# Kernel tuning notes

Hardware: AMD Instinct MI355X
Metric: run time of the kernel (lower is better)

Reference implementation:

```python
import jax, jax.numpy as jnp
import numpy as np

N0, N1, N2 = 20000, 15000, 15000
N = N0 + N1 + N2          # total nodes
E = 800000                # edges
H, D = 4, 64              # heads, hidden per head
ED = 64                   # edge feature dim
NET = 8                   # num edge types
C = 16                    # num classes
SLOPE = 0.2               # leaky relu negative slope
ALPHA = 0.05              # residual-attention mixing

def _glorot(key, shape):
    return jax.random.normal(key, shape, dtype=jnp.float32) / jnp.sqrt(jnp.float32(shape[-1]))

def setup_inputs() -> dict:
    key = jax.random.key(0)
    ks = jax.random.split(key, 32)
    return {
        "x0": jax.random.normal(ks[0], (N0, 128), jnp.float32),
        "x1": jax.random.normal(ks[1], (N1, 64), jnp.float32),
        "x2": jax.random.normal(ks[2], (N2, 32), jnp.float32),
        "src": jax.random.randint(ks[3], (E,), 0, N),
        "dst": jax.random.randint(ks[4], (E,), 0, N),
        "efeat": jax.random.randint(ks[5], (E,), 0, NET),
        # per-node-type input projections (fc_list)
        "W0": _glorot(ks[6], (64, 128)), "b0": jnp.zeros((64,), jnp.float32),
        "W1": _glorot(ks[7], (64, 64)),  "b1": jnp.zeros((64,), jnp.float32),
        "W2": _glorot(ks[8], (64, 32)),  "b2": jnp.zeros((64,), jnp.float32),
        # GAT layer 0: in 64 -> H*D, no residual, elu
        "Wg0": _glorot(ks[9], (H * D, 64)),
        "etab0": _glorot(ks[10], (NET, ED)),
        "We0": _glorot(ks[11], (H * ED, ED)),
        "al0": _glorot(ks[12], (H, D)), "ar0": _glorot(ks[13], (H, D)), "ae0": _glorot(ks[14], (H, ED)),
        # GAT layer 1: in H*D -> H*D, identity residual, elu
        "Wg1": _glorot(ks[15], (H * D, H * D)),
        "etab1": _glorot(ks[16], (NET, ED)),
        "We1": _glorot(ks[17], (H * ED, ED)),
        "al1": _glorot(ks[18], (H, D)), "ar1": _glorot(ks[19], (H, D)), "ae1": _glorot(ks[20], (H, ED)),
        # final GAT layer: in H*D -> 1*C, linear residual, no activation
        "Wg2": _glorot(ks[21], (C, H * D)),
        "etab2": _glorot(ks[22], (NET, ED)),
        "We2": _glorot(ks[23], (ED, ED)),
        "al2": _glorot(ks[24], (1, C)), "ar2": _glorot(ks[25], (1, C)), "ae2": _glorot(ks[26], (1, ED)),
        "resW2": _glorot(ks[27], (C, H * D)),
    }

def _edge_softmax(scores, dst):
    # softmax over incoming edges of each dst node; scores: [E, H]
    m = jax.ops.segment_max(scores, dst, num_segments=N)
    ex = jnp.exp(scores - m[dst])
    s = jax.ops.segment_sum(ex, dst, num_segments=N)
    return ex / (s[dst] + 1e-9)

def _gat_conv(h, src, dst, et, Wg, etab, We, al, ar, ae, res_attn, res, resW, act):
    nH, oD = al.shape
    feat = (h @ Wg.T).reshape(N, nH, oD)                 # [N,H,D]
    ee = (etab[et] @ We.T).reshape(E, nH, -1)            # [E,H,ED]
    el = jnp.einsum('nhd,hd->nh', feat, al)
    er = jnp.einsum('nhd,hd->nh', feat, ar)
    es = jnp.einsum('ehd,hd->eh', ee, ae)
    logits = jax.nn.leaky_relu(el[src] + er[dst] + es, SLOPE)
    a = _edge_softmax(logits, dst)                       # [E,H]
    if res_attn is not None:
        a = a * (1.0 - ALPHA) + res_attn * ALPHA
    out = jax.ops.segment_sum(a[:, :, None] * feat[src], dst, num_segments=N)
    if res:
        resval = (h @ resW.T).reshape(N, -1, oD) if resW is not None else h.reshape(N, nH, oD)
        out = out + resval
    if act is not None:
        out = act(out)
    return out, jax.lax.stop_gradient(a)                 # attention detached (res_attn)

def reference(x0, x1, x2, src, dst, efeat, W0, b0, W1, b1, W2, b2,
              Wg0, etab0, We0, al0, ar0, ae0,
              Wg1, etab1, We1, al1, ar1, ae1,
              Wg2, etab2, We2, al2, ar2, ae2, resW2):
    h = jnp.concatenate([x0 @ W0.T + b0, x1 @ W1.T + b1, x2 @ W2.T + b2], axis=0)  # [N,64]
    h, ra = _gat_conv(h, src, dst, efeat, Wg0, etab0, We0, al0, ar0, ae0, None, False, None, jax.nn.elu)
    h = h.reshape(N, -1)
    h, ra = _gat_conv(h, src, dst, efeat, Wg1, etab1, We1, al1, ar1, ae1, ra, True, None, jax.nn.elu)
    h = h.reshape(N, -1)
    logits, _ = _gat_conv(h, src, dst, efeat, Wg2, etab2, We2, al2, ar2, ae2, None, True, resW2, None)
    return logits.mean(axis=1)                           # [N, C]
```

## Files before the change

### kernel.cpp

```cpp
#include <hip/hip_runtime.h>
#include <math.h>

#define N0 20000
#define N1 15000
#define N2 15000
#define NN 50000
#define EE 800000
#define SLOPE 0.2f
#define ALPHA 0.05f

typedef _Float16 h8 __attribute__((ext_vector_type(8)));
typedef _Float16 h4 __attribute__((ext_vector_type(4)));
typedef float f4v __attribute__((ext_vector_type(4)));

__device__ __forceinline__ float sel4(float4 v, int h) {
    float lo = (h & 1) ? v.y : v.x;
    float hi = (h & 1) ? v.w : v.z;
    return (h & 2) ? hi : lo;
}

__device__ __forceinline__ float elu_fast(float x) {
    return x > 0.f ? x : __expf(x) - 1.f;
}


__device__ __forceinline__ void es_pair(int p,
                                        const float* __restrict__ etab0, const float* __restrict__ We0, const float* __restrict__ ae0,
                                        const float* __restrict__ etab1, const float* __restrict__ We1, const float* __restrict__ ae1,
                                        const float* __restrict__ etab2, const float* __restrict__ We2, const float* __restrict__ ae2,
                                        float* __restrict__ es) {
    const float *etab, *We, *ae;
    float* out;
    int H;
    if (p < 32)      { etab = etab0; We = We0; ae = ae0; out = es;      H = 4; }
    else if (p < 64) { p -= 32; etab = etab1; We = We1; ae = ae1; out = es + 32; H = 4; }
    else             { p -= 64; etab = etab2; We = We2; ae = ae2; out = es + 64; H = 1; }
    int t = p / H, h = p % H;
    int j = threadIdx.x & 63;
    const float* w = We + (size_t)(h * 64 + j) * 64;
    const float* e = etab + t * 64;
    float s = 0.f;
    #pragma unroll
    for (int k = 0; k < 64; k += 4) {
        float4 wv = *(const float4*)(w + k);
        float4 ev = *(const float4*)(e + k);
        s += wv.x * ev.x + wv.y * ev.y + wv.z * ev.z + wv.w * ev.w;
    }
    s *= ae[h * 64 + j];
    #pragma unroll
    for (int off = 32; off > 0; off >>= 1) s += __shfl_down(s, off);
    if (j == 0) out[t * H + h] = s;
}

__device__ __forceinline__ void cvt4(const float* __restrict__ s, _Float16* __restrict__ d, int t) {
    float4 v = ((const float4*)s)[t];
    h4 o;
    o[0] = (_Float16)v.x; o[1] = (_Float16)v.y;
    o[2] = (_Float16)v.z; o[3] = (_Float16)v.w;
    ((h4*)d)[t] = o;
}


__global__ __launch_bounds__(256) void k1_hist_prep(
        const int* __restrict__ dst, int* __restrict__ deg,
        const float* etab0, const float* We0, const float* ae0,
        const float* etab1, const float* We1, const float* ae1,
        const float* etab2, const float* We2, const float* ae2,
        float* es,
        const float* s0, _Float16* d0, int n0,
        const float* s1, _Float16* d1, int n1,
        const float* s2, _Float16* d2, int n2,
        const float* s3, _Float16* d3, int n3,
        const float* s4, _Float16* d4, int n4,
        const float* s5, _Float16* d5, int n5,
        const float* s6, _Float16* d6, int n6,
        const float* s7, _Float16* d7, int n7,
        const float* s8, _Float16* d8, int n8,
        const float* s9, _Float16* d9, int n9, int EB) {
    int b = blockIdx.x;
    if (b < EB) {
        int e = b * 256 + threadIdx.x;
        if (e < EE) atomicAdd(&deg[dst[e]], 1);
        return;
    }
    b -= EB;
    if (b < 18) {
        int p = b * 4 + (threadIdx.x >> 6);
        if (p < 72) es_pair(p, etab0, We0, ae0, etab1, We1, ae1, etab2, We2, ae2, es);
        return;
    }
    int t = (b - 18) * 256 + threadIdx.x;
    if (t < (n0 >> 2)) { cvt4(s0, d0, t); return; } t -= n0 >> 2;
    if (t < (n1 >> 2)) { cvt4(s1, d1, t); return; } t -= n1 >> 2;
    if (t < (n2 >> 2)) { cvt4(s2, d2, t); return; } t -= n2 >> 2;
    if (t < (n3 >> 2)) { cvt4(s3, d3, t); return; } t -= n3 >> 2;
    if (t < (n4 >> 2)) { cvt4(s4, d4, t); return; } t -= n4 >> 2;
    if (t < (n5 >> 2)) { cvt4(s5, d5, t); return; } t -= n5 >> 2;
    if (t < (n6 >> 2)) { cvt4(s6, d6, t); return; } t -= n6 >> 2;
    if (t < (n7 >> 2)) { cvt4(s7, d7, t); return; } t -= n7 >> 2;
    if (t < (n8 >> 2)) { cvt4(s8, d8, t); return; } t -= n8 >> 2;
    if (t < (n9 >> 2)) { cvt4(s9, d9, t); }
}


__device__ __forceinline__ void block_sum_body(int b, const int* __restrict__ deg,
                                               int* __restrict__ bsum, int n) {
    int i = b * 256 + threadIdx.x;
    int v = (i < n) ? deg[i] : 0;
    #pragma unroll
    for (int off = 32; off > 0; off >>= 1) v += __shfl_down(v, off);
    __shared__ int sh[4];
    if ((threadIdx.x & 63) == 0) sh[threadIdx.x >> 6] = v;
    __syncthreads();
    if (threadIdx.x == 0) bsum[b] = sh[0] + sh[1] + sh[2] + sh[3];
}

__global__ __launch_bounds__(256) void scan_out2(const int* __restrict__ deg,
                                                 const int* __restrict__ bsum,
                                                 int* __restrict__ rowstart,
                                                 int* __restrict__ cursor, int n, int nb) {
    __shared__ int sb[256];
    __shared__ int boff_s;
    int tid = threadIdx.x;
    int v = (tid < nb) ? bsum[tid] : 0;
    sb[tid] = v;
    __syncthreads();
    #pragma unroll
    for (int off = 1; off < 256; off <<= 1) {
        int t = (tid >= off) ? sb[tid - off] : 0;
        __syncthreads();
        sb[tid] += t;
        __syncthreads();
    }
    if (tid == blockIdx.x) boff_s = sb[tid] - v;
    __syncthreads();
    int boff = boff_s;
    int i = blockIdx.x * 256 + tid;
    int d = (i < n) ? deg[i] : 0;
    __syncthreads();
    sb[tid] = d;
    __syncthreads();
    #pragma unroll
    for (int off = 1; off < 256; off <<= 1) {
        int t = (tid >= off) ? sb[tid - off] : 0;
        __syncthreads();
        sb[tid] += t;
        __syncthreads();
    }
    int excl = sb[tid] - d + boff;
    if (i < n) { rowstart[i] = excl; cursor[i] = excl; }
    if (i == n - 1) rowstart[n] = excl + d;
}


template<int NT, int ELR>
__device__ __forceinline__ void gemm_body(int bx, int by,
                                          const _Float16* __restrict__ A,
                                          const _Float16* __restrict__ B,
                                          const float* __restrict__ bias,
                                          float* __restrict__ Cf,
                                          _Float16* __restrict__ Ch,
                                          float* __restrict__ el,
                                          float* __restrict__ er,
                                          const float* __restrict__ al,
                                          const float* __restrict__ ar,
                                          int M, int N, int K) {
    const int wave = threadIdx.x >> 6;
    const int lane = threadIdx.x & 63;
    const int m_base = (bx * 4 + wave) * 32;
    const int n_base = by * (NT * 16);
    const int row = lane & 15;
    const int kq = (lane >> 4) * 8;

    f4v acc[2][NT];
    #pragma unroll
    for (int i = 0; i < 2; i++)
        #pragma unroll
        for (int j = 0; j < NT; j++) {
            f4v z = {0.f, 0.f, 0.f, 0.f};
            acc[i][j] = z;
        }

    int ra = m_base + row;       if (ra >= M) ra = M - 1;
    int rb2 = m_base + 16 + row; if (rb2 >= M) rb2 = M - 1;
    const _Float16* a0p = A + (size_t)ra * K + kq;
    const _Float16* a1p = A + (size_t)rb2 * K + kq;
    const _Float16* bp  = B + (size_t)(n_base + row) * K + kq;

    for (int k = 0; k < K; k += 32) {
        h8 a0 = *(const h8*)(a0p + k);
        h8 a1 = *(const h8*)(a1p + k);
        #pragma unroll
        for (int j = 0; j < NT; j++) {
            h8 b = *(const h8*)(bp + (size_t)j * 16 * K + k);
            acc[0][j] = __builtin_amdgcn_mfma_f32_16x16x32_f16(a0, b, acc[0][j], 0, 0, 0);
            acc[1][j] = __builtin_amdgcn_mfma_f32_16x16x32_f16(a1, b, acc[1][j], 0, 0, 0);
        }
    }

    const int col = lane & 15;
    const int rb = (lane >> 4) * 4;

    if (ELR == 1) {
        float alw[NT], arw[NT];
        #pragma unroll
        for (int j = 0; j < NT; j++) {
            int cg = n_base + j * 16 + col;
            int hg = cg >> 6, d = cg & 63;
            alw[j] = al[hg * 64 + d];
            arw[j] = ar[hg * 64 + d];
        }
        const int hb = n_base >> 6;
        #pragma unroll
        for (int ms = 0; ms < 2; ms++) {
            #pragma unroll
            for (int r = 0; r < 4; r++) {
                float e0 = 0.f, e1 = 0.f, f0 = 0.f, f1 = 0.f;
                #pragma unroll
                for (int j = 0; j < NT; j++) {
                    float av = acc[ms][j][r];
                    if (j < NT / 2) { e0 = fmaf(av, alw[j], e0); f0 = fmaf(av, arw[j], f0); }
                    else            { e1 = fmaf(av, alw[j], e1); f1 = fmaf(av, arw[j], f1); }
                }
                #pragma unroll
                for (int off = 1; off <= 8; off <<= 1) {
                    e0 += __shfl_xor(e0, off);
                    e1 += __shfl_xor(e1, off);
                    f0 += __shfl_xor(f0, off);
                    f1 += __shfl_xor(f1, off);
                }
                int m = m_base + ms * 16 + rb + r;
                if (col == 0 && m < M) {
                    el[m * 4 + hb]     = e0;
                    el[m * 4 + hb + 1] = e1;
                    er[m * 4 + hb]     = f0;
                    er[m * 4 + hb + 1] = f1;
                }
            }
        }
    }
    if (ELR == 2) {
        float alw = al[col], arw = ar[col];
        #pragma unroll
        for (int ms = 0; ms < 2; ms++) {
            #pragma unroll
            for (int r = 0; r < 4; r++) {
                float e = acc[ms][0][r] * alw;
                float f = acc[ms][0][r] * arw;
                #pragma unroll
                for (int off = 1; off <= 8; off <<= 1) {
                    e += __shfl_xor(e, off);
                    f += __shfl_xor(f, off);
                }
                int m = m_base + ms * 16 + rb + r;
                if (col == 0 && m < M) { el[m] = e; er[m] = f; }
            }
        }
    }

    #pragma unroll
    for (int ms = 0; ms < 2; ms++) {
        #pragma unroll
        for (int j = 0; j < NT; j++) {
            #pragma unroll
            for (int r = 0; r < 4; r++) {
                int m = m_base + ms * 16 + rb + r;
                if (m < M) {
                    int n = n_base + j * 16 + col;
                    float v = acc[ms][j][r];
                    if (bias) v += bias[n];
                    if (Cf) Cf[(size_t)m * N + n] = v;
                    if (Ch) Ch[(size_t)m * N + n] = (_Float16)v;
                }
            }
        }
    }
}

template<int NT, int ELR>
__global__ __launch_bounds__(256) void gemm_mfma(const _Float16* __restrict__ A,
                                                 const _Float16* __restrict__ B,
                                                 const float* __restrict__ bias,
                                                 float* __restrict__ Cf,
                                                 _Float16* __restrict__ Ch,
                                                 float* __restrict__ el,
                                                 float* __restrict__ er,
                                                 const float* __restrict__ al,
                                                 const float* __restrict__ ar,
                                                 int M, int N, int K) {
    gemm_body<NT, ELR>(blockIdx.x, blockIdx.y, A, B, bias, Cf, Ch, el, er, al, ar, M, N, K);
}


__global__ __launch_bounds__(256) void k2_bsum_proj(
        const int* __restrict__ deg, int* __restrict__ bsum, int NBv,
        const _Float16* __restrict__ x0h, const _Float16* __restrict__ W0h, const float* __restrict__ b0,
        const _Float16* __restrict__ x1h, const _Float16* __restrict__ W1h, const float* __restrict__ b1,
        const _Float16* __restrict__ x2h, const _Float16* __restrict__ W2h, const float* __restrict__ b2,
        _Float16* __restrict__ h0h, int nb0, int nb1) {
    int b = blockIdx.x;
    if (b < NBv) { block_sum_body(b, deg, bsum, NN); return; }
    b -= NBv;
    if (b < nb0) {
        gemm_body<4, 0>(b, 0, x0h, W0h, b0, nullptr, h0h,
                        nullptr, nullptr, nullptr, nullptr, N0, 64, 128);
    } else if (b < nb0 + nb1) {
        gemm_body<4, 0>(b - nb0, 0, x1h, W1h, b1, nullptr, h0h + (size_t)N0 * 64,
                        nullptr, nullptr, nullptr, nullptr, N1, 64, 64);
    } else {
        gemm_body<4, 0>(b - nb0 - nb1, 0, x2h, W2h, b2, nullptr, h0h + (size_t)(N0 + N1) * 64,
                        nullptr, nullptr, nullptr, nullptr, N2, 64, 32);
    }
}


__global__ __launch_bounds__(256) void k4_scat_gemm0(
        const int* __restrict__ src, const int* __restrict__ dst, const int* __restrict__ et,
        int* __restrict__ cursor, int* __restrict__ pk, int EB,
        const _Float16* __restrict__ h0h, const _Float16* __restrict__ Wg0h,
        _Float16* __restrict__ feath, float* __restrict__ el, float* __restrict__ er,
        const float* __restrict__ al0, const float* __restrict__ ar0, int MB) {
    int b = blockIdx.x;
    if (b < EB) {
        int e = b * 256 + threadIdx.x;
        if (e < EE) {
            int d = dst[e];
            int p = atomicAdd(&cursor[d], 1);
            pk[p] = (et[e] << 16) | src[e];
        }
        return;
    }
    int t = b - EB;
    int bx = t % MB, by = t / MB;
    gemm_body<8, 1>(bx, by, h0h, Wg0h, nullptr, nullptr, feath, el, er, al0, ar0, NN, 256, 64);
}


template<bool WRITE_A, bool HAS_PREV, bool HAS_RES>
__global__ __launch_bounds__(256) void gat_fused4(const int* __restrict__ rowstart,
                                                  const int* __restrict__ pk,
                                                  const float* __restrict__ el,
                                                  const float* __restrict__ er,
                                                  const float* __restrict__ es,
                                                  const _Float16* __restrict__ feat,
                                                  const _Float16* __restrict__ aprev,
                                                  _Float16* __restrict__ awrite,
                                                  const _Float16* __restrict__ resh,
                                                  _Float16* __restrict__ outh, int nN) {
    __shared__ int2 as_lds[4][4][66];
    const int wave = threadIdx.x >> 6;
    const int lane = threadIdx.x & 63;
    int n = blockIdx.x * 4 + wave;
    if (n >= nN) return;
    const int r0 = rowstart[n], r1 = rowstart[n + 1];
    const int deg = r1 - r0;
    float4 er4 = *(const float4*)(er + n * 4);

    if (deg <= 64) {
        const int idx = r0 + lane;
        const bool act = idx < r1;
        int p = act ? pk[idx] : 0;
        int psrc = p & 0xFFFF;
        float4 v4 = {-INFINITY, -INFINITY, -INFINITY, -INFINITY};
        if (act) {
            float4 e4 = *(const float4*)(el + psrc * 4);
            float4 c4 = *(const float4*)(es + (p >> 16) * 4);
            float v;
            v = e4.x + er4.x + c4.x; v4.x = v > 0.f ? v : SLOPE * v;
            v = e4.y + er4.y + c4.y; v4.y = v > 0.f ? v : SLOPE * v;
            v = e4.z + er4.z + c4.z; v4.z = v > 0.f ? v : SLOPE * v;
            v = e4.w + er4.w + c4.w; v4.w = v > 0.f ? v : SLOPE * v;
        }
        float4 m4 = v4;
        #pragma unroll
        for (int off = 1; off <= 8; off <<= 1) {
            m4.x = fmaxf(m4.x, __shfl_xor(m4.x, off));
            m4.y = fmaxf(m4.y, __shfl_xor(m4.y, off));
            m4.z = fmaxf(m4.z, __shfl_xor(m4.z, off));
            m4.w = fmaxf(m4.w, __shfl_xor(m4.w, off));
        }
        if (deg > 16) {
            m4.x = fmaxf(m4.x, __shfl_xor(m4.x, 16));
            m4.y = fmaxf(m4.y, __shfl_xor(m4.y, 16));
            m4.z = fmaxf(m4.z, __shfl_xor(m4.z, 16));
            m4.w = fmaxf(m4.w, __shfl_xor(m4.w, 16));
        }
        if (deg > 32) {
            m4.x = fmaxf(m4.x, __shfl_xor(m4.x, 32));
            m4.y = fmaxf(m4.y, __shfl_xor(m4.y, 32));
            m4.z = fmaxf(m4.z, __shfl_xor(m4.z, 32));
            m4.w = fmaxf(m4.w, __shfl_xor(m4.w, 32));
        }
        float4 ex = {0.f, 0.f, 0.f, 0.f};
        if (act) {
            ex.x = __expf(v4.x - m4.x);
            ex.y = __expf(v4.y - m4.y);
            ex.z = __expf(v4.z - m4.z);
            ex.w = __expf(v4.w - m4.w);
        }
        float4 s4 = ex;
        #pragma unroll
        for (int off = 1; off <= 8; off <<= 1) {
            s4.x += __shfl_xor(s4.x, off);
            s4.y += __shfl_xor(s4.y, off);
            s4.z += __shfl_xor(s4.z, off);
            s4.w += __shfl_xor(s4.w, off);
        }
        if (deg > 16) {
            s4.x += __shfl_xor(s4.x, 16);
            s4.y += __shfl_xor(s4.y, 16);
            s4.z += __shfl_xor(s4.z, 16);
            s4.w += __shfl_xor(s4.w, 16);
        }
        if (deg > 32) {
            s4.x += __shfl_xor(s4.x, 32);
            s4.y += __shfl_xor(s4.y, 32);
            s4.z += __shfl_xor(s4.z, 32);
            s4.w += __shfl_xor(s4.w, 32);
        }
        float4 a4;
        a4.x = ex.x / (s4.x + 1e-9f);
        a4.y = ex.y / (s4.y + 1e-9f);
        a4.z = ex.z / (s4.z + 1e-9f);
        a4.w = ex.w / (s4.w + 1e-9f);
        if (HAS_PREV && act) {
            h4 pv = *(const h4*)(aprev + (size_t)idx * 4);
            a4.x = a4.x * (1.f - ALPHA) + ALPHA * (float)pv[0];
            a4.y = a4.y * (1.f - ALPHA) + ALPHA * (float)pv[1];
            a4.z = a4.z * (1.f - ALPHA) + ALPHA * (float)pv[2];
            a4.w = a4.w * (1.f - ALPHA) + ALPHA * (float)pv[3];
        }
        if (WRITE_A && act) {
            h4 aw;
            aw[0] = (_Float16)a4.x; aw[1] = (_Float16)a4.y;
            aw[2] = (_Float16)a4.z; aw[3] = (_Float16)a4.w;
            *(h4*)(awrite + (size_t)idx * 4) = aw;
        }
        as_lds[wave][0][lane] = make_int2(__float_as_int(a4.x), psrc);
        as_lds[wave][1][lane] = make_int2(__float_as_int(a4.y), psrc);
        as_lds[wave][2][lane] = make_int2(__float_as_int(a4.z), psrc);
        as_lds[wave][3][lane] = make_int2(__float_as_int(a4.w), psrc);

        const int half = lane >> 5;
        const int fl = lane & 31;
        const int h = fl >> 3;
        float acc8[8];
        #pragma unroll
        for (int q = 0; q < 8; q++) acc8[q] = 0.f;
        int i = r0;
        for (; i + 7 < r1; i += 8) {
            int j0 = (i - r0) + half;
            int2 e0 = as_lds[wave][h][j0 + 0];
            int2 e1 = as_lds[wave][h][j0 + 2];
            int2 e2 = as_lds[wave][h][j0 + 4];
            int2 e3 = as_lds[wave][h][j0 + 6];
            float a0 = __int_as_float(e0.x), a1 = __int_as_float(e1.x);
            float a2 = __int_as_float(e2.x), a3 = __int_as_float(e3.x);
            h8 f0 = *(const h8*)(feat + (size_t)e0.y * 256 + fl * 8);
            h8 f1 = *(const h8*)(feat + (size_t)e1.y * 256 + fl * 8);
            h8 f2 = *(const h8*)(feat + (size_t)e2.y * 256 + fl * 8);
            h8 f3 = *(const h8*)(feat + (size_t)e3.y * 256 + fl * 8);
            #pragma unroll
            for (int q = 0; q < 8; q++) acc8[q] = fmaf(a0, (float)f0[q], acc8[q]);
            #pragma unroll
            for (int q = 0; q < 8; q++) acc8[q] = fmaf(a1, (float)f1[q], acc8[q]);
            #pragma unroll
            for (int q = 0; q < 8; q++) acc8[q] = fmaf(a2, (float)f2[q], acc8[q]);
            #pragma unroll
            for (int q = 0; q < 8; q++) acc8[q] = fmaf(a3, (float)f3[q], acc8[q]);
        }
        for (; i + 3 < r1; i += 4) {
            int j0 = (i - r0) + half;
            int2 e0 = as_lds[wave][h][j0 + 0];
            int2 e1 = as_lds[wave][h][j0 + 2];
            float a0 = __int_as_float(e0.x), a1 = __int_as_float(e1.x);
            h8 f0 = *(const h8*)(feat + (size_t)e0.y * 256 + fl * 8);
            h8 f1 = *(const h8*)(feat + (size_t)e1.y * 256 + fl * 8);
            #pragma unroll
            for (int q = 0; q < 8; q++) acc8[q] = fmaf(a0, (float)f0[q], acc8[q]);
            #pragma unroll
            for (int q = 0; q < 8; q++) acc8[q] = fmaf(a1, (float)f1[q], acc8[q]);
        }
        for (; i + 1 < r1; i += 2) {
            int j0 = (i - r0) + half;
            int2 e0 = as_lds[wave][h][j0];
            float a0 = __int_as_float(e0.x);
            h8 f0 = *(const h8*)(feat + (size_t)e0.y * 256 + fl * 8);
            #pragma unroll
            for (int q = 0; q < 8; q++) acc8[q] = fmaf(a0, (float)f0[q], acc8[q]);
        }
        if (i < r1) {
            int j0 = i - r0;
            int2 e0 = as_lds[wave][h][j0];
            float a0 = (half == 0) ? __int_as_float(e0.x) : 0.f;
            h8 f0 = *(const h8*)(feat + (size_t)e0.y * 256 + fl * 8);
            #pragma unroll
            for (int q = 0; q < 8; q++) acc8[q] = fmaf(a0, (float)f0[q], acc8[q]);
        }
        #pragma unroll
        for (int q = 0; q < 8; q++) acc8[q] += __shfl_xor(acc8[q], 32);

        if (half == 0) {
            if (HAS_RES) {
                h8 rv = *(const h8*)(resh + (size_t)n * 256 + fl * 8);
                #pragma unroll
                for (int q = 0; q < 8; q++) acc8[q] += (float)rv[q];
            }
            #pragma unroll
            for (int q = 0; q < 8; q++) acc8[q] = elu_fast(acc8[q]);
            h8 o;
            #pragma unroll
            for (int q = 0; q < 8; q++) o[q] = (_Float16)acc8[q];
            *(h8*)(outh + (size_t)n * 256 + fl * 8) = o;
        }
        return;
    }

    float4 m4 = {-INFINITY, -INFINITY, -INFINITY, -INFINITY};
    for (int base = r0; base < r1; base += 64) {
        int idx = base + lane;
        if (idx < r1) {
            int p = pk[idx];
            float4 e4 = *(const float4*)(el + (p & 0xFFFF) * 4);
            float4 c4 = *(const float4*)(es + (p >> 16) * 4);
            float v;
            v = e4.x + er4.x + c4.x; v = v > 0.f ? v : SLOPE * v; m4.x = fmaxf(m4.x, v);
            v = e4.y + er4.y + c4.y; v = v > 0.f ? v : SLOPE * v; m4.y = fmaxf(m4.y, v);
            v = e4.z + er4.z + c4.z; v = v > 0.f ? v : SLOPE * v; m4.z = fmaxf(m4.z, v);
            v = e4.w + er4.w + c4.w; v = v > 0.f ? v : SLOPE * v; m4.w = fmaxf(m4.w, v);
        }
    }
    #pragma unroll
    for (int off = 1; off < 64; off <<= 1) {
        m4.x = fmaxf(m4.x, __shfl_xor(m4.x, off));
        m4.y = fmaxf(m4.y, __shfl_xor(m4.y, off));
        m4.z = fmaxf(m4.z, __shfl_xor(m4.z, off));
        m4.w = fmaxf(m4.w, __shfl_xor(m4.w, off));
    }
    float4 s4 = {0.f, 0.f, 0.f, 0.f};
    for (int base = r0; base < r1; base += 64) {
        int idx = base + lane;
        if (idx < r1) {
            int p = pk[idx];
            float4 e4 = *(const float4*)(el + (p & 0xFFFF) * 4);
            float4 c4 = *(const float4*)(es + (p >> 16) * 4);
            float4 exv;
            float v;
            v = e4.x + er4.x + c4.x; v = v > 0.f ? v : SLOPE * v; exv.x = __expf(v - m4.x);
            v = e4.y + er4.y + c4.y; v = v > 0.f ? v : SLOPE * v; exv.y = __expf(v - m4.y);
            v = e4.z + er4.z + c4.z; v = v > 0.f ? v : SLOPE * v; exv.z = __expf(v - m4.z);
            v = e4.w + er4.w + c4.w; v = v > 0.f ? v : SLOPE * v; exv.w = __expf(v - m4.w);
            if (base == r0) {
                as_lds[wave][0][lane] = make_int2(__float_as_int(exv.x), p & 0xFFFF);
                as_lds[wave][1][lane] = make_int2(__float_as_int(exv.y), p & 0xFFFF);
                as_lds[wave][2][lane] = make_int2(__float_as_int(exv.z), p & 0xFFFF);
                as_lds[wave][3][lane] = make_int2(__float_as_int(exv.w), p & 0xFFFF);
            }
            s4.x += exv.x; s4.y += exv.y; s4.z += exv.z; s4.w += exv.w;
        }
    }
    #pragma unroll
    for (int off = 1; off < 64; off <<= 1) {
        s4.x += __shfl_xor(s4.x, off);
        s4.y += __shfl_xor(s4.y, off);
        s4.z += __shfl_xor(s4.z, off);
        s4.w += __shfl_xor(s4.w, off);
    }
    float4 inv4;
    inv4.x = 1.f / (s4.x + 1e-9f); inv4.y = 1.f / (s4.y + 1e-9f);
    inv4.z = 1.f / (s4.z + 1e-9f); inv4.w = 1.f / (s4.w + 1e-9f);
    {
        int idx = r0 + lane;
        float4 a;
        a.x = __int_as_float(as_lds[wave][0][lane].x) * inv4.x;
        a.y = __int_as_float(as_lds[wave][1][lane].x) * inv4.y;
        a.z = __int_as_float(as_lds[wave][2][lane].x) * inv4.z;
        a.w = __int_as_float(as_lds[wave][3][lane].x) * inv4.w;
        if (HAS_PREV) {
            h4 pv = *(const h4*)(aprev + (size_t)idx * 4);
            a.x = a.x * (1.f - ALPHA) + ALPHA * (float)pv[0];
            a.y = a.y * (1.f - ALPHA) + ALPHA * (float)pv[1];
            a.z = a.z * (1.f - ALPHA) + ALPHA * (float)pv[2];
            a.w = a.w * (1.f - ALPHA) + ALPHA * (float)pv[3];
        }
        if (WRITE_A) {
            h4 aw;
            aw[0] = (_Float16)a.x; aw[1] = (_Float16)a.y;
            aw[2] = (_Float16)a.z; aw[3] = (_Float16)a.w;
            *(h4*)(awrite + (size_t)idx * 4) = aw;
        }
        as_lds[wave][0][lane].x = __float_as_int(a.x);
        as_lds[wave][1][lane].x = __float_as_int(a.y);
        as_lds[wave][2][lane].x = __float_as_int(a.z);
        as_lds[wave][3][lane].x = __float_as_int(a.w);
    }
    if (WRITE_A) {
        for (int base = r0 + 64; base < r1; base += 64) {
            int idx = base + lane;
            if (idx < r1) {
                int p = pk[idx];
                float4 e4 = *(const float4*)(el + (p & 0xFFFF) * 4);
                float4 c4 = *(const float4*)(es + (p >> 16) * 4);
                float4 a;
                float v;
                v = e4.x + er4.x + c4.x; v = v > 0.f ? v : SLOPE * v; a.x = __expf(v - m4.x) * inv4.x;
                v = e4.y + er4.y + c4.y; v = v > 0.f ? v : SLOPE * v; a.y = __expf(v - m4.y) * inv4.y;
                v = e4.z + er4.z + c4.z; v = v > 0.f ? v : SLOPE * v; a.z = __expf(v - m4.z) * inv4.z;
                v = e4.w + er4.w + c4.w; v = v > 0.f ? v : SLOPE * v; a.w = __expf(v - m4.w) * inv4.w;
                if (HAS_PREV) {
                    h4 pv = *(const h4*)(aprev + (size_t)idx * 4);
                    a.x = a.x * (1.f - ALPHA) + ALPHA * (float)pv[0];
                    a.y = a.y * (1.f - ALPHA) + ALPHA * (float)pv[1];
                    a.z = a.z * (1.f - ALPHA) + ALPHA * (float)pv[2];
                    a.w = a.w * (1.f - ALPHA) + ALPHA * (float)pv[3];
                }
                h4 aw;
                aw[0] = (_Float16)a.x; aw[1] = (_Float16)a.y;
                aw[2] = (_Float16)a.z; aw[3] = (_Float16)a.w;
                *(h4*)(awrite + (size_t)idx * 4) = aw;
            }
        }
    }
    const int h = lane >> 4;
    float4 acc = {0.f, 0.f, 0.f, 0.f};
    const int cap = r0 + 64;
    for (int i = r0; i < cap; i++) {
        int2 e0 = as_lds[wave][h][i - r0];
        h4 f = *(const h4*)(feat + (size_t)e0.y * 256 + lane * 4);
        float av = __int_as_float(e0.x);
        acc.x = fmaf(av, (float)f[0], acc.x);
        acc.y = fmaf(av, (float)f[1], acc.y);
        acc.z = fmaf(av, (float)f[2], acc.z);
        acc.w = fmaf(av, (float)f[3], acc.w);
    }
    {
        float mh = sel4(m4, h), invh = sel4(inv4, h), erh = sel4(er4, h);
        for (int i = cap; i < r1; i++) {
            int p = pk[i];
            int s = p & 0xFFFF, t = p >> 16;
            float v = el[s * 4 + h] + erh + es[t * 4 + h];
            v = v > 0.f ? v : SLOPE * v;
            float a = __expf(v - mh) * invh;
            if (HAS_PREV) a = a * (1.f - ALPHA) + ALPHA * (float)aprev[(size_t)i * 4 + h];
            h4 f = *(const h4*)(feat + (size_t)s * 256 + lane * 4);
            acc.x = fmaf(a, (float)f[0], acc.x);
            acc.y = fmaf(a, (float)f[1], acc.y);
            acc.z = fmaf(a, (float)f[2], acc.z);
            acc.w = fmaf(a, (float)f[3], acc.w);
        }
    }
    if (HAS_RES) {
        h4 rv = *(const h4*)(resh + (size_t)n * 256 + lane * 4);
        acc.x += (float)rv[0]; acc.y += (float)rv[1];
        acc.z += (float)rv[2]; acc.w += (float)rv[3];
    }
    acc.x = elu_fast(acc.x);
    acc.y = elu_fast(acc.y);
    acc.z = elu_fast(acc.z);
    acc.w = elu_fast(acc.w);
    h4 o;
    o[0] = (_Float16)acc.x; o[1] = (_Float16)acc.y;
    o[2] = (_Float16)acc.z; o[3] = (_Float16)acc.w;
    *(h4*)(outh + (size_t)n * 256 + lane * 4) = o;
}


__global__ __launch_bounds__(256) void gat_fused1(const int* __restrict__ rowstart,
                                                  const int* __restrict__ pk,
                                                  const float* __restrict__ el,
                                                  const float* __restrict__ er,
                                                  const float* __restrict__ es,
                                                  const _Float16* __restrict__ cpack,
                                                  float* __restrict__ out, int nN) {
    const int wave = threadIdx.x >> 6;
    const int lane = threadIdx.x & 63;
    int n = blockIdx.x * 4 + wave;
    if (n >= nN) return;
    const int r0 = rowstart[n], r1 = rowstart[n + 1];
    const int deg = r1 - r0;
    const float ern = er[n];

    if (deg <= 64) {
        const int idx = r0 + lane;
        const bool act = idx < r1;
        int p = act ? pk[idx] : 0;
        int psrc = p & 0xFFFF;
        float v = -INFINITY;
        if (act) {
            float t = el[psrc] + ern + es[p >> 16];
            v = t > 0.f ? t : SLOPE * t;
        }
        float m = v;
        #pragma unroll
        for (int off = 1; off <= 8; off <<= 1) m = fmaxf(m, __shfl_xor(m, off));
        if (deg > 16) m = fmaxf(m, __shfl_xor(m, 16));
        if (deg > 32) m = fmaxf(m, __shfl_xor(m, 32));
        float ex = act ? __expf(v - m) : 0.f;
        float s = ex;
        #pragma unroll
        for (int off = 1; off <= 8; off <<= 1) s += __shfl_xor(s, off);
        if (deg > 16) s += __shfl_xor(s, 16);
        if (deg > 32) s += __shfl_xor(s, 32);
        float a = ex / (s + 1e-9f);

        const int eslot = lane >> 4, fl = lane & 15;
        float acc = 0.f;
        int i = r0;
        for (; i + 7 < r1; i += 8) {
            int j0 = (i - r0) + eslot;
            int j1 = j0 + 4;
            int s0 = __shfl(psrc, j0);
            int s1 = __shfl(psrc, j1);
            float a0 = __shfl(a, j0);
            float a1 = __shfl(a, j1);
            float f0 = (float)cpack[(size_t)s0 * 32 + fl];
            float f1 = (float)cpack[(size_t)s1 * 32 + fl];
            acc = fmaf(a0, f0, acc);
            acc = fmaf(a1, f1, acc);
        }
        for (; i + 3 < r1; i += 4) {
            int j = (i - r0) + eslot;
            int sj = __shfl(psrc, j);
            float aj = __shfl(a, j);
            acc = fmaf(aj, (float)cpack[(size_t)sj * 32 + fl], acc);
        }
        int rem = r1 - i;
        if (rem > 0) {
            int j = (i - r0) + (eslot < rem ? eslot : rem - 1);
            int sj = __shfl(psrc, j);
            float aj = __shfl(a, j);
            if (eslot >= rem) aj = 0.f;
            acc = fmaf(aj, (float)cpack[(size_t)sj * 32 + fl], acc);
        }
        acc += __shfl_xor(acc, 16);
        acc += __shfl_xor(acc, 32);
        if (lane < 16) out[(size_t)n * 16 + lane] = acc + (float)cpack[(size_t)n * 32 + 16 + lane];
        return;
    }

    float m = -INFINITY;
    for (int base = r0; base < r1; base += 64) {
        int idx = base + lane;
        if (idx < r1) {
            int p = pk[idx];
            float v = el[p & 0xFFFF] + ern + es[p >> 16];
            v = v > 0.f ? v : SLOPE * v;
            m = fmaxf(m, v);
        }
    }
    #pragma unroll
    for (int off = 1; off < 64; off <<= 1) m = fmaxf(m, __shfl_xor(m, off));
    float s = 0.f;
    for (int base = r0; base < r1; base += 64) {
        int idx = base + lane;
        if (idx < r1) {
            int p = pk[idx];
            float v = el[p & 0xFFFF] + ern + es[p >> 16];
            v = v > 0.f ? v : SLOPE * v;
            s += __expf(v - m);
        }
    }
    #pragma unroll
    for (int off = 1; off < 64; off <<= 1) s += __shfl_xor(s, off);
    float inv = 1.f / (s + 1e-9f);
    const int eslot = lane >> 4, fl = lane & 15;
    float acc = 0.f;
    for (int i = r0; i < r1; i += 4) {
        int rem = r1 - i;
        if (eslot < rem) {
            int j = i + eslot;
            int p = pk[j];
            float v = el[p & 0xFFFF] + ern + es[p >> 16];
            v = v > 0.f ? v : SLOPE * v;
            float a = __expf(v - m) * inv;
            acc = fmaf(a, (float)cpack[(size_t)(p & 0xFFFF) * 32 + fl], acc);
        }
    }
    acc += __shfl_xor(acc, 16);
    acc += __shfl_xor(acc, 32);
    if (lane < 16) out[(size_t)n * 16 + lane] = acc + (float)cpack[(size_t)n * 32 + 16 + lane];
}


extern "C" void kernel_launch(void* const* d_in, const int* in_sizes, int n_in,
                              void* d_out, int out_size, void* d_ws, size_t ws_size,
                              hipStream_t stream) {
    const float* x0 = (const float*)d_in[0];
    const float* x1 = (const float*)d_in[1];
    const float* x2 = (const float*)d_in[2];
    const int* src  = (const int*)d_in[3];
    const int* dst  = (const int*)d_in[4];
    const int* et   = (const int*)d_in[5];
    const float* W0 = (const float*)d_in[6];  const float* b0 = (const float*)d_in[7];
    const float* W1 = (const float*)d_in[8];  const float* b1 = (const float*)d_in[9];
    const float* W2 = (const float*)d_in[10]; const float* b2 = (const float*)d_in[11];
    const float* Wg0 = (const float*)d_in[12]; const float* etab0 = (const float*)d_in[13];
    const float* We0 = (const float*)d_in[14]; const float* al0 = (const float*)d_in[15];
    const float* ar0 = (const float*)d_in[16]; const float* ae0 = (const float*)d_in[17];
    const float* Wg1 = (const float*)d_in[18]; const float* etab1 = (const float*)d_in[19];
    const float* We1 = (const float*)d_in[20]; const float* al1 = (const float*)d_in[21];
    const float* ar1 = (const float*)d_in[22]; const float* ae1 = (const float*)d_in[23];
    const float* Wg2 = (const float*)d_in[24]; const float* etab2 = (const float*)d_in[25];
    const float* We2 = (const float*)d_in[26]; const float* al2 = (const float*)d_in[27];
    const float* ar2 = (const float*)d_in[28]; const float* ae2 = (const float*)d_in[29];
    const float* resW2 = (const float*)d_in[30];
    float* outp = (float*)d_out;

    char* p = (char*)d_ws;
    auto alloc = [&](size_t bytes) -> void* {
        void* r = (void*)p;
        p += (bytes + 255) & ~(size_t)255;
        return r;
    };
    _Float16* x0h   = (_Float16*)alloc((size_t)N0 * 128 * 2);
    _Float16* x1h   = (_Float16*)alloc((size_t)N1 * 64 * 2);
    _Float16* x2h   = (_Float16*)alloc((size_t)N2 * 32 * 2);
    _Float16* W0h   = (_Float16*)alloc(64 * 128 * 2);
    _Float16* W1h   = (_Float16*)alloc(64 * 64 * 2);
    _Float16* W2h   = (_Float16*)alloc(64 * 32 * 2);
    _Float16* Wg0h  = (_Float16*)alloc(256 * 64 * 2);
    _Float16* Wg1h  = (_Float16*)alloc(256 * 256 * 2);
    _Float16* wpkh  = (_Float16*)alloc(32 * 256 * 2);
    _Float16* h0h   = (_Float16*)alloc((size_t)NN * 64 * 2);
    _Float16* feath = (_Float16*)alloc((size_t)NN * 256 * 2);
    _Float16* bufAh = (_Float16*)alloc((size_t)NN * 256 * 2);
    _Float16* bufBh = (_Float16*)alloc((size_t)NN * 256 * 2);
    _Float16* a0h   = (_Float16*)alloc((size_t)EE * 4 * 2);
    _Float16* cpackh = (_Float16*)alloc((size_t)NN * 32 * 2);
    float* el    = (float*)alloc((size_t)NN * 4 * 4);
    float* er    = (float*)alloc((size_t)NN * 4 * 4);
    float* es    = (float*)alloc(96 * 4);
    int* rowstart = (int*)alloc((size_t)(NN + 1) * 4);
    int* deg      = (int*)alloc((size_t)NN * 4);
    int* cursor   = (int*)alloc((size_t)NN * 4);
    int* bsum     = (int*)alloc(256 * 4);
    int* pk       = (int*)alloc((size_t)EE * 4);

    const int EB = (EE + 255) / 256;
    const int NB = (NN + 255) / 256;
    const int MB128 = (NN + 127) / 128;
    const int WB = (NN + 3) / 4;
    const int nb0 = (N0 + 127) / 128;
    const int nb1 = (N1 + 127) / 128;
    const int nb2 = (N2 + 127) / 128;

    hipMemsetAsync(deg, 0, (size_t)NN * 4, stream);

    {
        int n0c = N0 * 128, n1c = N1 * 64, n2c = N2 * 32;
        int total4 = (n0c + n1c + n2c + 8192 + 4096 + 2048 + 16384 + 65536 + 4096 + 4096) / 4;
        int cvb = (total4 + 255) / 256;
        k1_hist_prep<<<EB + 18 + cvb, 256, 0, stream>>>(
            dst, deg,
            etab0, We0, ae0, etab1, We1, ae1, etab2, We2, ae2, es,
            x0, x0h, n0c, x1, x1h, n1c, x2, x2h, n2c,
            W0, W0h, 8192, W1, W1h, 4096, W2, W2h, 2048,
            Wg0, Wg0h, 16384, Wg1, Wg1h, 65536,
            Wg2, wpkh, 4096, resW2, wpkh + 4096, 4096, EB);
    }

    k2_bsum_proj<<<NB + nb0 + nb1 + nb2, 256, 0, stream>>>(
        deg, bsum, NB, x0h, W0h, b0, x1h, W1h, b1, x2h, W2h, b2, h0h, nb0, nb1);

    scan_out2<<<NB, 256, 0, stream>>>(deg, bsum, rowstart, cursor, NN, NB);

    k4_scat_gemm0<<<EB + MB128 * 2, 256, 0, stream>>>(
        src, dst, et, cursor, pk, EB,
        h0h, Wg0h, feath, el, er, al0, ar0, MB128);

    gat_fused4<true, false, false><<<WB, 256, 0, stream>>>(
        rowstart, pk, el, er, es + 0, feath, nullptr, a0h, nullptr, bufAh, NN);

    gemm_mfma<8, 1><<<dim3(MB128, 2), 256, 0, stream>>>(bufAh, Wg1h, nullptr, nullptr, feath,
                                                        el, er, al1, ar1, NN, 256, 256);
    gat_fused4<false, true, true><<<WB, 256, 0, stream>>>(
        rowstart, pk, el, er, es + 32, feath, a0h, nullptr, bufAh, bufBh, NN);

    gemm_mfma<2, 2><<<dim3(MB128, 1), 256, 0, stream>>>(bufBh, wpkh, nullptr, nullptr, cpackh,
                                                        el, er, al2, ar2, NN, 32, 256);
    gat_fused1<<<WB, 256, 0, stream>>>(rowstart, pk, el, er, es + 64, cpackh, outp, NN);
}
```

Before: 464.6 us.

## Partition degree histogram and edge scatter by destination range to localize atomics

```diff
diff --git a/kernel.cpp b/kernel.cpp
--- a/kernel.cpp
+++ b/kernel.cpp
@@ -8,6 +8,9 @@
 #define EE 800000
 #define SLOPE 0.2f
 #define ALPHA 0.05f
+#define NODES_PER_G 6250
+#define HSLICE 64
+#define ECHUNK 12500
 
 typedef _Float16 h8 __attribute__((ext_vector_type(8)));
 typedef _Float16 h4 __attribute__((ext_vector_type(4)));
@@ -76,14 +79,19 @@
         const float* s6, _Float16* d6, int n6,
         const float* s7, _Float16* d7, int n7,
         const float* s8, _Float16* d8, int n8,
-        const float* s9, _Float16* d9, int n9, int EB) {
+        const float* s9, _Float16* d9, int n9) {
     int b = blockIdx.x;
-    if (b < EB) {
-        int e = b * 256 + threadIdx.x;
-        if (e < EE) atomicAdd(&deg[dst[e]], 1);
+    if (b < 8 * HSLICE) {
+        int g = b & 7, sl = b >> 3;
+        int lo = g * NODES_PER_G, hi = lo + NODES_PER_G;
+        int e0 = sl * ECHUNK, e1 = e0 + ECHUNK;
+        for (int e = e0 + threadIdx.x; e < e1; e += 256) {
+            int d = dst[e];
+            if (d >= lo && d < hi) atomicAdd(&deg[d], 1);
+        }
         return;
     }
-    b -= EB;
+    b -= 8 * HSLICE;
     if (b < 18) {
         int p = b * 4 + (threadIdx.x >> 6);
         if (p < 72) es_pair(p, etab0, We0, ae0, etab1, We1, ae1, etab2, We2, ae2, es);
@@ -316,21 +324,25 @@
 
 __global__ __launch_bounds__(256) void k4_scat_gemm0(
         const int* __restrict__ src, const int* __restrict__ dst, const int* __restrict__ et,
-        int* __restrict__ cursor, int* __restrict__ pk, int EB,
+        int* __restrict__ cursor, int* __restrict__ pk,
         const _Float16* __restrict__ h0h, const _Float16* __restrict__ Wg0h,
         _Float16* __restrict__ feath, float* __restrict__ el, float* __restrict__ er,
         const float* __restrict__ al0, const float* __restrict__ ar0, int MB) {
     int b = blockIdx.x;
-    if (b < EB) {
-        int e = b * 256 + threadIdx.x;
-        if (e < EE) {
+    if (b < 8 * HSLICE) {
+        int g = b & 7, sl = b >> 3;
+        int lo = g * NODES_PER_G, hi = lo + NODES_PER_G;
+        int e0 = sl * ECHUNK, e1 = e0 + ECHUNK;
+        for (int e = e0 + threadIdx.x; e < e1; e += 256) {
             int d = dst[e];
-            int p = atomicAdd(&cursor[d], 1);
-            pk[p] = (et[e] << 16) | src[e];
+            if (d >= lo && d < hi) {
+                int p = atomicAdd(&cursor[d], 1);
+                pk[p] = (et[e] << 16) | src[e];
+            }
         }
         return;
     }
-    int t = b - EB;
+    int t = b - 8 * HSLICE;
     int bx = t % MB, by = t / MB;
     gemm_body<8, 1>(bx, by, h0h, Wg0h, nullptr, nullptr, feath, el, er, al0, ar0, NN, 256, 64);
 }
@@ -836,13 +848,13 @@
     int* bsum     = (int*)alloc(256 * 4);
     int* pk       = (int*)alloc((size_t)EE * 4);
 
-    const int EB = (EE + 255) / 256;
     const int NB = (NN + 255) / 256;
     const int MB128 = (NN + 127) / 128;
     const int WB = (NN + 3) / 4;
     const int nb0 = (N0 + 127) / 128;
     const int nb1 = (N1 + 127) / 128;
     const int nb2 = (N2 + 127) / 128;
+    const int SB = 8 * HSLICE;
 
     hipMemsetAsync(deg, 0, (size_t)NN * 4, stream);
 
@@ -850,13 +862,13 @@
         int n0c = N0 * 128, n1c = N1 * 64, n2c = N2 * 32;
         int total4 = (n0c + n1c + n2c + 8192 + 4096 + 2048 + 16384 + 65536 + 4096 + 4096) / 4;
         int cvb = (total4 + 255) / 256;
-        k1_hist_prep<<<EB + 18 + cvb, 256, 0, stream>>>(
+        k1_hist_prep<<<SB + 18 + cvb, 256, 0, stream>>>(
             dst, deg,
             etab0, We0, ae0, etab1, We1, ae1, etab2, We2, ae2, es,
             x0, x0h, n0c, x1, x1h, n1c, x2, x2h, n2c,
             W0, W0h, 8192, W1, W1h, 4096, W2, W2h, 2048,
             Wg0, Wg0h, 16384, Wg1, Wg1h, 65536,
-            Wg2, wpkh, 4096, resW2, wpkh + 4096, 4096, EB);
+            Wg2, wpkh, 4096, resW2, wpkh + 4096, 4096);
     }
 
     k2_bsum_proj<<<NB + nb0 + nb1 + nb2, 256, 0, stream>>>(
@@ -864,8 +876,8 @@
 
     scan_out2<<<NB, 256, 0, stream>>>(deg, bsum, rowstart, cursor, NN, NB);
 
-    k4_scat_gemm0<<<EB + MB128 * 2, 256, 0, stream>>>(
-        src, dst, et, cursor, pk, EB,
+    k4_scat_gemm0<<<SB + MB128 * 2, 256, 0, stream>>>(
+        src, dst, et, cursor, pk,
         h0h, Wg0h, feath, el, er, al0, ar0, MB128);
 
     gat_fused4<true, false, false><<<WB, 256, 0, stream>>>(
```

After: 447.9 us. 1.04x faster.
